# Performance work log

Measured on AMD Instinct MI355X. Metric: run time of the kernel, lower is better.

Reference implementation:

```python
import jax, jax.numpy as jnp
import numpy as np
from functools import partial

# dims matching init_kwargs
H = 512      # hidden_size
F = 2048     # ff_size
NH = 8       # num_heads
NL = 6       # num_layers
V = 1024     # vocab_size
T = 8        # sentence_length
S = 5        # n_sentences_in_paragraph
P = 16       # n_paragraphs_in_article
L = P * S * T          # article_length = 640
N = L + 1              # sequence length used by masks = 641
B = 16                 # batch
HD = H // NH           # head dim
LN_EPS = 1e-5
NEG = -1e9


def _build_mask():
    # pseudo_causal_masks[0] from the torch __init__: causal ~tril plus
    # blocking of within-paragraph sentence-0 key columns.
    a = np.ones((P, S, T, P, S, T), dtype=bool)
    j = np.arange(P)
    a[j, :, :, j, 0, :] = False
    a = a.reshape(L, L)
    causal = ~np.tril(np.ones((N, N), dtype=bool))
    m = causal.copy()
    m[:-1, 1:] = np.logical_and(a, causal[:-1, 1:])
    return m  # True = disallowed


def _build_pe():
    # sinusoidal pe exactly as in __init__ (div_term uses hidden_size in denom)
    pos = np.arange(N, dtype=np.float32)[:, None]
    div = np.exp(np.arange(0, H // 2, dtype=np.float32) * (-np.log(10000.0) / H))
    pe = np.zeros((N, H), dtype=np.float32)
    pe[:, 0::2] = np.sin(pos * div)
    pe[:, 1::2] = np.cos(pos * div)
    return pe


def setup_inputs() -> dict:
    key = jax.random.key(0)
    ks = jax.random.split(key, 12)
    sd = 0.02
    inp = {
        'tokens': jax.random.randint(ks[0], (B, N), 0, V),
        'attn_mask': jnp.asarray(_build_mask()),
        'pe': jnp.asarray(_build_pe()),
        'emb': jax.random.normal(ks[1], (V, H), jnp.float32) * sd,
        'qkv_w': jax.random.normal(ks[2], (NL, 3 * H, H), jnp.float32) * sd,
        'qkv_b': jnp.zeros((NL, 3 * H), jnp.float32),
        'out_w': jax.random.normal(ks[3], (NL, H, H), jnp.float32) * sd,
        'out_b': jnp.zeros((NL, H), jnp.float32),
        'ln1_g': jnp.ones((NL, H), jnp.float32),
        'ln1_b': jnp.zeros((NL, H), jnp.float32),
        'fc1_w': jax.random.normal(ks[4], (NL, F, H), jnp.float32) * sd,
        'fc1_b': jnp.zeros((NL, F), jnp.float32),
        'fc2_w': jax.random.normal(ks[5], (NL, H, F), jnp.float32) * sd,
        'fc2_b': jnp.zeros((NL, H), jnp.float32),
        'ln2_g': jnp.ones((NL, H), jnp.float32),
        'ln2_b': jnp.zeros((NL, H), jnp.float32),
        'lnf_g': jnp.ones((H,), jnp.float32),
        'lnf_b': jnp.zeros((H,), jnp.float32),
        'dep_w': jax.random.normal(ks[6], (V, H), jnp.float32) * sd,
        'dep_b': jnp.zeros((V,), jnp.float32),
    }
    return inp


def _ln(x, g, b):
    m = jnp.mean(x, axis=-1, keepdims=True)
    v = jnp.mean(jnp.square(x - m), axis=-1, keepdims=True)
    return (x - m) * jax.lax.rsqrt(v + LN_EPS) * g + b


def _encoder_layer(x, p, mask):
    qw, qb, ow, ob, g1, b1, w1, bb1, w2, bb2, g2, b2 = p
    Bsz, Nn, _ = x.shape
    qkv = x @ qw.T + qb                                   # [B,N,3H]
    q, k, v = jnp.split(qkv, 3, axis=-1)
    q = q.reshape(Bsz, Nn, NH, HD)
    k = k.reshape(Bsz, Nn, NH, HD)
    v = v.reshape(Bsz, Nn, NH, HD)
    scores = jnp.einsum('bqhd,bkhd->bhqk', q, k) / jnp.sqrt(jnp.asarray(HD, x.dtype))
    scores = jnp.where(mask[None, None], NEG, scores)
    att = jax.nn.softmax(scores, axis=-1)
    o = jnp.einsum('bhqk,bkhd->bqhd', att, v).reshape(Bsz, Nn, H)
    o = o @ ow.T + ob
    x = _ln(x + o, g1, b1)                                # post-LN (torch default)
    f = jax.nn.gelu(x @ w1.T + bb1, approximate=False) @ w2.T + bb2
    return _ln(x + f, g2, b2)


def reference(tokens, attn_mask, pe, emb, qkv_w, qkv_b, out_w, out_b,
              ln1_g, ln1_b, fc1_w, fc1_b, fc2_w, fc2_b, ln2_g, ln2_b,
              lnf_g, lnf_b, dep_w, dep_b):
    x = emb[tokens] + pe[None]                            # [B,N,H]
    layers = (qkv_w, qkv_b, out_w, out_b, ln1_g, ln1_b,
              fc1_w, fc1_b, fc2_w, fc2_b, ln2_g, ln2_b)

    def step(h, p):
        return _encoder_layer(h, p, attn_mask), None

    x, _ = jax.lax.scan(step, x, layers)
    x = _ln(x, lnf_g, lnf_b)
    return x @ dep_w.T + dep_b                            # [B,N,V] logits
```

## Files before the change

### kernel.cpp

```cpp
#include <hip/hip_runtime.h>
#include <stdint.h>

#define NSEQ 641
#define BATCH 16
#define MROWS (BATCH * NSEQ)
#define HID 512
#define FFD 2048
#define NHEAD 8
#define HDIM 64
#define NLAYER 6
#define VOCAB 1024

typedef __bf16 bf16x8 __attribute__((ext_vector_type(8)));
typedef float  f32x4  __attribute__((ext_vector_type(4)));
typedef int    i32x4  __attribute__((ext_vector_type(4)));
typedef short  s16x8  __attribute__((ext_vector_type(8)));
typedef short  s16x4  __attribute__((ext_vector_type(4)));

__device__ __forceinline__ uint32_t swz(uint32_t b) { return b ^ (((b >> 7) & 7u) << 4); }

__device__ __forceinline__ unsigned short f2bf(float f) {
  uint32_t u = __builtin_bit_cast(uint32_t, f);
  u += 0x7FFFu + ((u >> 16) & 1u);
  return (unsigned short)(u >> 16);
}

__device__ __forceinline__ void gload16(const void* g, void* l) {
  __builtin_amdgcn_global_load_lds(
      (const __attribute__((address_space(1))) uint32_t*)g,
      (__attribute__((address_space(3))) uint32_t*)l, 16, 0, 0);
}

__device__ __forceinline__ bf16x8 ld_lds16(const void* p) {
  return __builtin_bit_cast(bf16x8, *(const i32x4*)p);
}

__global__ void cvt_kernel(const float* __restrict__ in,
                           unsigned short* __restrict__ out, int n) {
  int i = (blockIdx.x * 256 + threadIdx.x) * 4;
  if (i >= n) return;
  f32x4 v = *(const f32x4*)(in + i);
  s16x4 o;
  o[0] = (short)f2bf(v[0]); o[1] = (short)f2bf(v[1]);
  o[2] = (short)f2bf(v[2]); o[3] = (short)f2bf(v[3]);
  *(s16x4*)(out + i) = o;
}

__global__ void embed_kernel(const int* __restrict__ tok,
                             const float* __restrict__ emb,
                             const float* __restrict__ pe,
                             float* __restrict__ x,
                             unsigned short* __restrict__ xb) {
  int m = blockIdx.x;
  int n = m % NSEQ;
  int t = tok[m];
  int h = threadIdx.x * 4;
  f32x4 e = *(const f32x4*)(emb + (size_t)t * HID + h);
  f32x4 p = *(const f32x4*)(pe + (size_t)n * HID + h);
  f32x4 v = e + p;
  *(f32x4*)(x + (size_t)m * HID + h) = v;
  s16x4 o;
  o[0] = (short)f2bf(v[0]); o[1] = (short)f2bf(v[1]);
  o[2] = (short)f2bf(v[2]); o[3] = (short)f2bf(v[3]);
  *(s16x4*)(xb + (size_t)m * HID + h) = o;
}

__global__ __launch_bounds__(256) void ln_kernel(
    const float* __restrict__ in, const float* __restrict__ gg,
    const float* __restrict__ bb, float* __restrict__ xo,
    unsigned short* __restrict__ xbo, int rows) {
  int row = blockIdx.x * 4 + (threadIdx.x >> 6);
  if (row >= rows) return;
  int lane = threadIdx.x & 63;
  const float* p = in + (size_t)row * HID + lane * 8;
  f32x4 a0 = *(const f32x4*)p;
  f32x4 a1 = *(const f32x4*)(p + 4);
  float s = a0[0] + a0[1] + a0[2] + a0[3] + a1[0] + a1[1] + a1[2] + a1[3];
#pragma unroll
  for (int o = 32; o; o >>= 1) s += __shfl_xor(s, o);
  float mean = s * (1.0f / HID);
  float vs = 0.f;
#pragma unroll
  for (int j = 0; j < 4; ++j) { float d = a0[j] - mean; vs += d * d; }
#pragma unroll
  for (int j = 0; j < 4; ++j) { float d = a1[j] - mean; vs += d * d; }
#pragma unroll
  for (int o = 32; o; o >>= 1) vs += __shfl_xor(vs, o);
  float rstd = rsqrtf(vs * (1.0f / HID) + 1e-5f);
  f32x4 g0 = *(const f32x4*)(gg + lane * 8);
  f32x4 g1 = *(const f32x4*)(gg + lane * 8 + 4);
  f32x4 b0 = *(const f32x4*)(bb + lane * 8);
  f32x4 b1 = *(const f32x4*)(bb + lane * 8 + 4);
  f32x4 y0, y1;
  s16x8 ob;
#pragma unroll
  for (int j = 0; j < 4; ++j) {
    y0[j] = (a0[j] - mean) * rstd * g0[j] + b0[j];
    y1[j] = (a1[j] - mean) * rstd * g1[j] + b1[j];
    ob[j] = (short)f2bf(y0[j]);
    ob[j + 4] = (short)f2bf(y1[j]);
  }
  float* xp = xo + (size_t)row * HID + lane * 8;
  *(f32x4*)xp = y0;
  *(f32x4*)(xp + 4) = y1;
  *(s16x8*)(xbo + (size_t)row * HID + lane * 8) = ob;
}

enum { EPI_QKV = 0, EPI_GELU = 1, EPI_RESID = 2, EPI_F32OUT = 3 };

template <int EPI>
__global__ __launch_bounds__(256, 2) void gemm_bt(
    const unsigned short* __restrict__ A, const unsigned short* __restrict__ W,
    const float* __restrict__ bias, const float* __restrict__ resid,
    void* __restrict__ out0, void* __restrict__ out1, void* __restrict__ out2,
    int M, int N, int K) {
  __shared__ char sm[32768];
  const int tid = threadIdx.x, lane = tid & 63, wid = tid >> 6;
  const int wr = wid >> 1, wc = wid & 1;
  const int m0 = blockIdx.y * 128, n0 = blockIdx.x * 128;
  f32x4 acc[4][4] = {};
  const uint32_t Pbase = wid * 4096;

  for (int kt = 0; kt < K; kt += 64) {
#pragma unroll
    for (int i = 0; i < 4; ++i) {
      uint32_t P = Pbase + i * 1024 + lane * 16;
      uint32_t L = swz(P);
      int row = (int)(L >> 7);
      uint32_t kb = L & 127u;
      int ma = m0 + row; if (ma >= M) ma = M - 1;
      gload16((const char*)A + ((size_t)ma * K + kt) * 2 + kb, sm + Pbase + i * 1024);
      gload16((const char*)W + ((size_t)(n0 + row) * K + kt) * 2 + kb,
              sm + 16384 + Pbase + i * 1024);
    }
    __syncthreads();
#pragma unroll
    for (int kk = 0; kk < 2; ++kk) {
      bf16x8 af[4], bfr[4];
#pragma unroll
      for (int mi = 0; mi < 4; ++mi) {
        int row = wr * 64 + mi * 16 + (lane & 15);
        af[mi] = ld_lds16(sm + swz((uint32_t)row * 128 + kk * 64 + ((lane >> 4) << 4)));
      }
#pragma unroll
      for (int ni = 0; ni < 4; ++ni) {
        int row = wc * 64 + ni * 16 + (lane & 15);
        bfr[ni] = ld_lds16(sm + 16384 + swz((uint32_t)row * 128 + kk * 64 + ((lane >> 4) << 4)));
      }
#pragma unroll
      for (int mi = 0; mi < 4; ++mi)
#pragma unroll
        for (int ni = 0; ni < 4; ++ni)
          acc[mi][ni] = __builtin_amdgcn_mfma_f32_16x16x32_bf16(af[mi], bfr[ni], acc[mi][ni], 0, 0, 0);
    }
    __syncthreads();
  }

#pragma unroll
  for (int mi = 0; mi < 4; ++mi) {
#pragma unroll
    for (int g = 0; g < 4; ++g) {
      int m = m0 + wr * 64 + mi * 16 + (lane >> 4) * 4 + g;
      if (m >= M) continue;
      int bbq = 0, nn = 0;
      if (EPI == EPI_QKV) { bbq = m / NSEQ; nn = m - bbq * NSEQ; }
#pragma unroll
      for (int ni = 0; ni < 4; ++ni) {
        int c = n0 + wc * 64 + ni * 16 + (lane & 15);
        float v = acc[mi][ni][g] + bias[c];
        if (EPI == EPI_QKV) {
          int which = c >> 9, hh = (c >> 6) & 7, d = c & 63;
          unsigned short* dst = which == 0 ? (unsigned short*)out0
                              : which == 1 ? (unsigned short*)out1
                                           : (unsigned short*)out2;
          dst[(((size_t)bbq * NHEAD + hh) * NSEQ + nn) * HDIM + d] = f2bf(v);
        } else if (EPI == EPI_GELU) {
          v = 0.5f * v * (1.0f + erff(v * 0.70710678118654752f));
          ((unsigned short*)out0)[(size_t)m * N + c] = f2bf(v);
        } else if (EPI == EPI_RESID) {
          float* o = (float*)out0;
          o[(size_t)m * N + c] = v + resid[(size_t)m * N + c];
        } else {
          ((float*)out0)[(size_t)m * N + c] = v;
        }
      }
    }
  }
}

__global__ __launch_bounds__(256) void attn_kernel(
    const unsigned short* __restrict__ Q, const unsigned short* __restrict__ Kb,
    const unsigned short* __restrict__ V, unsigned short* __restrict__ O) {
  const int qt = blockIdx.x, bh = blockIdx.y;
  const int b = bh >> 3, h = bh & 7;
  const int q0 = qt * 64;
  const int tid = threadIdx.x, lane = tid & 63, w = tid >> 6;
  __shared__ char sK[8192];
  __shared__ char sV[8192];
  __shared__ char sP[4][2048];

  const size_t base = (size_t)bh * (NSEQ * HDIM);

  bf16x8 qf[2];
  {
    int qr = q0 + w * 16 + (lane & 15);
    if (qr > NSEQ - 1) qr = NSEQ - 1;
#pragma unroll
    for (int kk = 0; kk < 2; ++kk)
      qf[kk] = __builtin_bit_cast(
          bf16x8, *(const i32x4*)(Q + base + (size_t)qr * HDIM + kk * 32 + ((lane >> 4) << 3)));
  }

  f32x4 acc[4] = {};
  float mrow[4] = {-1e30f, -1e30f, -1e30f, -1e30f};
  float lrow[4] = {0.f, 0.f, 0.f, 0.f};
  const int qrow_base = q0 + w * 16 + ((lane >> 4) << 2);

  int nkt = (q0 + 103) / 64 + 1;
  if (nkt > 11) nkt = 11;

  for (int kt = 0; kt < nkt; ++kt) {
    const int k0 = kt * 64;
#pragma unroll
    for (int i = 0; i < 2; ++i) {
      uint32_t P = w * 2048 + i * 1024 + lane * 16;
      uint32_t L = swz(P);
      int row = (int)(L >> 7);
      uint32_t kbyte = L & 127u;
      int kr = k0 + row; if (kr > NSEQ - 1) kr = NSEQ - 1;
      gload16((const char*)(Kb + base + (size_t)kr * HDIM) + kbyte, sK + w * 2048 + i * 1024);
    }
#pragma unroll
    for (int it = 0; it < 2; ++it) {
      int idx = it * 256 + tid;
      int key = idx >> 3, d0 = (idx & 7) << 3;
      int kr = k0 + key; if (kr > NSEQ - 1) kr = NSEQ - 1;
      s16x8 vv = *(const s16x8*)(V + base + (size_t)kr * HDIM + d0);
#pragma unroll
      for (int j = 0; j < 8; ++j)
        *(short*)(sV + swz((uint32_t)(d0 + j) * 128 + key * 2)) = vv[j];
    }
    __syncthreads();

    f32x4 s[4] = {};
#pragma unroll
    for (int nt = 0; nt < 4; ++nt) {
#pragma unroll
      for (int kk = 0; kk < 2; ++kk) {
        int row = nt * 16 + (lane & 15);
        bf16x8 kf = ld_lds16(sK + swz((uint32_t)row * 128 + kk * 64 + ((lane >> 4) << 4)));
        s[nt] = __builtin_amdgcn_mfma_f32_16x16x32_bf16(qf[kk], kf, s[nt], 0, 0, 0);
      }
    }
    float mx[4];
#pragma unroll
    for (int g = 0; g < 4; ++g) {
      int q = qrow_base + g;
      int p = q / 40;
      int lo = p * 40 + 1, hi = p * 40 + 8;
      float best = -1e30f;
#pragma unroll
      for (int nt = 0; nt < 4; ++nt) {
        int k = k0 + nt * 16 + (lane & 15);
        bool ok = ((k <= q) || (k >= lo && k <= hi)) && (k < NSEQ);
        float v = ok ? s[nt][g] * 0.125f : -1e30f;
        s[nt][g] = v;
        best = fmaxf(best, v);
      }
      mx[g] = best;
    }
#pragma unroll
    for (int o = 1; o < 16; o <<= 1)
#pragma unroll
      for (int g = 0; g < 4; ++g) mx[g] = fmaxf(mx[g], __shfl_xor(mx[g], o));

    float alpha[4], rs[4];
#pragma unroll
    for (int g = 0; g < 4; ++g) {
      float mnew = fmaxf(mrow[g], mx[g]);
      alpha[g] = __expf(mrow[g] - mnew);
      mrow[g] = mnew;
      float sum = 0.f;
#pragma unroll
      for (int nt = 0; nt < 4; ++nt) {
        float pv = __expf(s[nt][g] - mnew);
        s[nt][g] = pv;
        sum += pv;
      }
      rs[g] = sum;
    }
#pragma unroll
    for (int o = 1; o < 16; o <<= 1)
#pragma unroll
      for (int g = 0; g < 4; ++g) rs[g] += __shfl_xor(rs[g], o);
#pragma unroll
    for (int g = 0; g < 4; ++g) {
      lrow[g] = lrow[g] * alpha[g] + rs[g];
#pragma unroll
      for (int nt = 0; nt < 4; ++nt) acc[nt][g] *= alpha[g];
    }

#pragma unroll
    for (int g = 0; g < 4; ++g) {
      int row = ((lane >> 4) << 2) + g;
#pragma unroll
      for (int nt = 0; nt < 4; ++nt) {
        int col = nt * 16 + (lane & 15);
        *(short*)(sP[w] + swz((uint32_t)row * 128 + col * 2)) = (short)f2bf(s[nt][g]);
      }
    }
#pragma unroll
    for (int kk = 0; kk < 2; ++kk) {
      int rowp = lane & 15;
      bf16x8 pa = ld_lds16(sP[w] + swz((uint32_t)rowp * 128 + kk * 64 + ((lane >> 4) << 4)));
#pragma unroll
      for (int nt = 0; nt < 4; ++nt) {
        int rowv = nt * 16 + (lane & 15);
        bf16x8 vf = ld_lds16(sV + swz((uint32_t)rowv * 128 + kk * 64 + ((lane >> 4) << 4)));
        acc[nt] = __builtin_amdgcn_mfma_f32_16x16x32_bf16(pa, vf, acc[nt], 0, 0, 0);
      }
    }
    __syncthreads();
  }

#pragma unroll
  for (int g = 0; g < 4; ++g) {
    int q = qrow_base + g;
    if (q >= NSEQ) continue;
    float inv = 1.0f / lrow[g];
#pragma unroll
    for (int nt = 0; nt < 4; ++nt) {
      int d = nt * 16 + (lane & 15);
      O[((size_t)b * NSEQ + q) * HID + h * HDIM + d] = f2bf(acc[nt][g] * inv);
    }
  }
}

extern "C" void kernel_launch(void* const* d_in, const int* in_sizes, int n_in,
                              void* d_out, int out_size, void* d_ws, size_t ws_size,
                              hipStream_t stream) {
  const int*   tok   = (const int*)d_in[0];
  const float* pe    = (const float*)d_in[2];
  const float* emb   = (const float*)d_in[3];
  const float* qkv_w = (const float*)d_in[4];
  const float* qkv_b = (const float*)d_in[5];
  const float* out_w = (const float*)d_in[6];
  const float* out_b = (const float*)d_in[7];
  const float* ln1_g = (const float*)d_in[8];
  const float* ln1_b = (const float*)d_in[9];
  const float* fc1_w = (const float*)d_in[10];
  const float* fc1_b = (const float*)d_in[11];
  const float* fc2_w = (const float*)d_in[12];
  const float* fc2_b = (const float*)d_in[13];
  const float* ln2_g = (const float*)d_in[14];
  const float* ln2_b = (const float*)d_in[15];
  const float* lnf_g = (const float*)d_in[16];
  const float* lnf_b = (const float*)d_in[17];
  const float* dep_w = (const float*)d_in[18];
  const float* dep_b = (const float*)d_in[19];

  char* w = (char*)d_ws;
  float* x = (float*)w;            w += (size_t)MROWS * HID * 4;
  unsigned short* xb = (unsigned short*)w; w += (size_t)MROWS * HID * 2;
  unsigned short* qb = (unsigned short*)w; w += (size_t)BATCH * NHEAD * NSEQ * HDIM * 2;
  unsigned short* kb = (unsigned short*)w; w += (size_t)BATCH * NHEAD * NSEQ * HDIM * 2;
  unsigned short* vb = (unsigned short*)w; w += (size_t)BATCH * NHEAD * NSEQ * HDIM * 2;
  unsigned short* ao = (unsigned short*)w; w += (size_t)BATCH * NHEAD * NSEQ * HDIM * 2;
  unsigned short* mid = qb;
  unsigned short* wl_qkv = (unsigned short*)w; w += (size_t)1536 * 512 * 2;
  unsigned short* wl_out = (unsigned short*)w; w += (size_t)512 * 512 * 2;
  unsigned short* wl_fc1 = (unsigned short*)w; w += (size_t)2048 * 512 * 2;
  unsigned short* wl_fc2 = (unsigned short*)w; w += (size_t)512 * 2048 * 2;
  unsigned short* wd     = (unsigned short*)w; w += (size_t)VOCAB * 512 * 2;

  cvt_kernel<<<dim3((VOCAB * 512) / 1024), 256, 0, stream>>>(dep_w, wd, VOCAB * 512);
  embed_kernel<<<dim3(MROWS), 128, 0, stream>>>(tok, emb, pe, x, xb);

  const int lnBlocks = (MROWS + 3) / 4;
  for (int l = 0; l < NLAYER; ++l) {
    cvt_kernel<<<dim3((1536 * 512) / 1024), 256, 0, stream>>>(qkv_w + (size_t)l * 1536 * 512, wl_qkv, 1536 * 512);
    cvt_kernel<<<dim3((512 * 512) / 1024), 256, 0, stream>>>(out_w + (size_t)l * 512 * 512, wl_out, 512 * 512);
    cvt_kernel<<<dim3((2048 * 512) / 1024), 256, 0, stream>>>(fc1_w + (size_t)l * 2048 * 512, wl_fc1, 2048 * 512);
    cvt_kernel<<<dim3((512 * 2048) / 1024), 256, 0, stream>>>(fc2_w + (size_t)l * 512 * 2048, wl_fc2, 512 * 2048);

    gemm_bt<EPI_QKV><<<dim3(12, 81), 256, 0, stream>>>(
        xb, wl_qkv, qkv_b + l * 1536, nullptr, qb, kb, vb, MROWS, 1536, 512);
    attn_kernel<<<dim3(11, 128), 256, 0, stream>>>(qb, kb, vb, ao);
    gemm_bt<EPI_RESID><<<dim3(4, 81), 256, 0, stream>>>(
        ao, wl_out, out_b + l * 512, x, x, nullptr, nullptr, MROWS, 512, 512);
    ln_kernel<<<dim3(lnBlocks), 256, 0, stream>>>(x, ln1_g + l * 512, ln1_b + l * 512, x, xb, MROWS);
    gemm_bt<EPI_GELU><<<dim3(16, 81), 256, 0, stream>>>(
        xb, wl_fc1, fc1_b + l * 2048, nullptr, mid, nullptr, nullptr, MROWS, 2048, 512);
    gemm_bt<EPI_RESID><<<dim3(4, 81), 256, 0, stream>>>(
        mid, wl_fc2, fc2_b + l * 512, x, x, nullptr, nullptr, MROWS, 512, 2048);
    ln_kernel<<<dim3(lnBlocks), 256, 0, stream>>>(x, ln2_g + l * 512, ln2_b + l * 512, x, xb, MROWS);
  }

  ln_kernel<<<dim3(lnBlocks), 256, 0, stream>>>(x, lnf_g, lnf_b, x, xb, MROWS);
  gemm_bt<EPI_F32OUT><<<dim3(8, 81), 256, 0, stream>>>(
      xb, wd, dep_b, nullptr, d_out, nullptr, nullptr, MROWS, VOCAB, 512);
}
```

Baseline: 1.598 ms.

## Pre-transpose V into padded layout and batch weight conversions upfront

Adds a vtrans kernel that writes V transposed into a [bh][d][KPAD] buffer, so the attention kernel can load V tiles with async global-to-LDS copies instead of scattered per-element LDS stores. When workspace allows, it also converts all layers' weights to bf16 in a few large launches before the layer loop instead of four small conversions per layer. This adds one extra kernel launch and an extra V read/write pass per layer, and uses more workspace.

New measurement: 1.507 ms. -5.7%, faster.

```diff
diff --git a/kernel.cpp b/kernel.cpp
--- a/kernel.cpp
+++ b/kernel.cpp
@@ -10,6 +10,7 @@
 #define HDIM 64
 #define NLAYER 6
 #define VOCAB 1024
+#define KPAD 704
 
 typedef __bf16 bf16x8 __attribute__((ext_vector_type(8)));
 typedef float  f32x4  __attribute__((ext_vector_type(4)));
@@ -104,6 +105,37 @@
   *(f32x4*)xp = y0;
   *(f32x4*)(xp + 4) = y1;
   *(s16x8*)(xbo + (size_t)row * HID + lane * 8) = ob;
+}
+
+__global__ __launch_bounds__(256) void vtrans_kernel(
+    const unsigned short* __restrict__ V, unsigned short* __restrict__ vT) {
+  const int kt = blockIdx.x;
+  const int bh = blockIdx.y;
+  const int k0 = kt * 64;
+  const int tid = threadIdx.x;
+  __shared__ unsigned short lds[64][68];
+  const size_t src = (size_t)bh * (NSEQ * HDIM);
+#pragma unroll
+  for (int it = 0; it < 2; ++it) {
+    int k = it * 32 + (tid >> 3);
+    int d0 = (tid & 7) * 8;
+    int kr = k0 + k;
+    s16x8 v = {};
+    if (kr < NSEQ) v = *(const s16x8*)(V + src + (size_t)kr * HDIM + d0);
+    *(s16x8*)&lds[k][d0] = v;
+  }
+  __syncthreads();
+  const int d = tid & 63;
+  const int w = tid >> 6;
+  const size_t dst = ((size_t)bh * 64 + d) * KPAD + k0;
+#pragma unroll
+  for (int it = 0; it < 2; ++it) {
+    int kc = w + it * 4;
+    s16x8 o;
+#pragma unroll
+    for (int i = 0; i < 8; ++i) o[i] = lds[kc * 8 + i][d];
+    *(s16x8*)(vT + dst + kc * 8) = o;
+  }
 }
 
 enum { EPI_QKV = 0, EPI_GELU = 1, EPI_RESID = 2, EPI_F32OUT = 3 };
@@ -190,31 +222,33 @@
 
 __global__ __launch_bounds__(256) void attn_kernel(
     const unsigned short* __restrict__ Q, const unsigned short* __restrict__ Kb,
-    const unsigned short* __restrict__ V, unsigned short* __restrict__ O) {
+    const unsigned short* __restrict__ vT, unsigned short* __restrict__ O) {
   const int qt = blockIdx.x, bh = blockIdx.y;
   const int b = bh >> 3, h = bh & 7;
   const int q0 = qt * 64;
   const int tid = threadIdx.x, lane = tid & 63, w = tid >> 6;
+  const int lg = lane >> 4, lc = lane & 15;
   __shared__ char sK[8192];
   __shared__ char sV[8192];
   __shared__ char sP[4][2048];
 
   const size_t base = (size_t)bh * (NSEQ * HDIM);
+  const size_t baseT = (size_t)bh * (HDIM * KPAD);
 
   bf16x8 qf[2];
   {
-    int qr = q0 + w * 16 + (lane & 15);
+    int qr = q0 + w * 16 + lc;
     if (qr > NSEQ - 1) qr = NSEQ - 1;
 #pragma unroll
     for (int kk = 0; kk < 2; ++kk)
       qf[kk] = __builtin_bit_cast(
-          bf16x8, *(const i32x4*)(Q + base + (size_t)qr * HDIM + kk * 32 + ((lane >> 4) << 3)));
+          bf16x8, *(const i32x4*)(Q + base + (size_t)qr * HDIM + kk * 32 + (lg << 3)));
   }
 
   f32x4 acc[4] = {};
   float mrow[4] = {-1e30f, -1e30f, -1e30f, -1e30f};
   float lrow[4] = {0.f, 0.f, 0.f, 0.f};
-  const int qrow_base = q0 + w * 16 + ((lane >> 4) << 2);
+  const int qrow_base = q0 + w * 16 + (lg << 2);
 
   int nkt = (q0 + 103) / 64 + 1;
   if (nkt > 11) nkt = 11;
@@ -231,14 +265,13 @@
       gload16((const char*)(Kb + base + (size_t)kr * HDIM) + kbyte, sK + w * 2048 + i * 1024);
     }
 #pragma unroll
-    for (int it = 0; it < 2; ++it) {
-      int idx = it * 256 + tid;
-      int key = idx >> 3, d0 = (idx & 7) << 3;
-      int kr = k0 + key; if (kr > NSEQ - 1) kr = NSEQ - 1;
-      s16x8 vv = *(const s16x8*)(V + base + (size_t)kr * HDIM + d0);
-#pragma unroll
-      for (int j = 0; j < 8; ++j)
-        *(short*)(sV + swz((uint32_t)(d0 + j) * 128 + key * 2)) = vv[j];
+    for (int i = 0; i < 2; ++i) {
+      uint32_t P = w * 2048 + i * 1024 + lane * 16;
+      uint32_t L = swz(P);
+      int drow = (int)(L >> 7);
+      uint32_t kbyte = L & 127u;
+      gload16((const char*)(vT + baseT + (size_t)drow * KPAD + k0) + kbyte,
+              sV + w * 2048 + i * 1024);
     }
     __syncthreads();
 
@@ -247,8 +280,8 @@
     for (int nt = 0; nt < 4; ++nt) {
 #pragma unroll
       for (int kk = 0; kk < 2; ++kk) {
-        int row = nt * 16 + (lane & 15);
-        bf16x8 kf = ld_lds16(sK + swz((uint32_t)row * 128 + kk * 64 + ((lane >> 4) << 4)));
+        int row = nt * 16 + lc;
+        bf16x8 kf = ld_lds16(sK + swz((uint32_t)row * 128 + kk * 64 + (lg << 4)));
         s[nt] = __builtin_amdgcn_mfma_f32_16x16x32_bf16(qf[kk], kf, s[nt], 0, 0, 0);
       }
     }
@@ -261,7 +294,7 @@
       float best = -1e30f;
 #pragma unroll
       for (int nt = 0; nt < 4; ++nt) {
-        int k = k0 + nt * 16 + (lane & 15);
+        int k = k0 + nt * 16 + lc;
         bool ok = ((k <= q) || (k >= lo && k <= hi)) && (k < NSEQ);
         float v = ok ? s[nt][g] * 0.125f : -1e30f;
         s[nt][g] = v;
@@ -302,21 +335,20 @@
 
 #pragma unroll
     for (int g = 0; g < 4; ++g) {
-      int row = ((lane >> 4) << 2) + g;
+      int row = (lg << 2) + g;
 #pragma unroll
       for (int nt = 0; nt < 4; ++nt) {
-        int col = nt * 16 + (lane & 15);
+        int col = nt * 16 + lc;
         *(short*)(sP[w] + swz((uint32_t)row * 128 + col * 2)) = (short)f2bf(s[nt][g]);
       }
     }
 #pragma unroll
     for (int kk = 0; kk < 2; ++kk) {
-      int rowp = lane & 15;
-      bf16x8 pa = ld_lds16(sP[w] + swz((uint32_t)rowp * 128 + kk * 64 + ((lane >> 4) << 4)));
+      bf16x8 pa = ld_lds16(sP[w] + swz((uint32_t)lc * 128 + kk * 64 + (lg << 4)));
 #pragma unroll
       for (int nt = 0; nt < 4; ++nt) {
-        int rowv = nt * 16 + (lane & 15);
-        bf16x8 vf = ld_lds16(sV + swz((uint32_t)rowv * 128 + kk * 64 + ((lane >> 4) << 4)));
+        int rowv = nt * 16 + lc;
+        bf16x8 vf = ld_lds16(sV + swz((uint32_t)rowv * 128 + kk * 64 + (lg << 4)));
         acc[nt] = __builtin_amdgcn_mfma_f32_16x16x32_bf16(pa, vf, acc[nt], 0, 0, 0);
       }
     }
@@ -330,7 +362,7 @@
     float inv = 1.0f / lrow[g];
 #pragma unroll
     for (int nt = 0; nt < 4; ++nt) {
-      int d = nt * 16 + (lane & 15);
+      int d = nt * 16 + lc;
       O[((size_t)b * NSEQ + q) * HID + h * HDIM + d] = f2bf(acc[nt][g] * inv);
     }
   }
@@ -359,6 +391,12 @@
   const float* dep_w = (const float*)d_in[18];
   const float* dep_b = (const float*)d_in[19];
 
+  const size_t SZ_QKV = (size_t)1536 * 512;
+  const size_t SZ_OUT = (size_t)512 * 512;
+  const size_t SZ_FC1 = (size_t)2048 * 512;
+  const size_t SZ_FC2 = (size_t)512 * 2048;
+  const size_t SZ_DEP = (size_t)VOCAB * 512;
+
   char* w = (char*)d_ws;
   float* x = (float*)w;            w += (size_t)MROWS * HID * 4;
   unsigned short* xb = (unsigned short*)w; w += (size_t)MROWS * HID * 2;
@@ -367,32 +405,60 @@
   unsigned short* vb = (unsigned short*)w; w += (size_t)BATCH * NHEAD * NSEQ * HDIM * 2;
   unsigned short* ao = (unsigned short*)w; w += (size_t)BATCH * NHEAD * NSEQ * HDIM * 2;
   unsigned short* mid = qb;
-  unsigned short* wl_qkv = (unsigned short*)w; w += (size_t)1536 * 512 * 2;
-  unsigned short* wl_out = (unsigned short*)w; w += (size_t)512 * 512 * 2;
-  unsigned short* wl_fc1 = (unsigned short*)w; w += (size_t)2048 * 512 * 2;
-  unsigned short* wl_fc2 = (unsigned short*)w; w += (size_t)512 * 2048 * 2;
-  unsigned short* wd     = (unsigned short*)w; w += (size_t)VOCAB * 512 * 2;
-
-  cvt_kernel<<<dim3((VOCAB * 512) / 1024), 256, 0, stream>>>(dep_w, wd, VOCAB * 512);
+  unsigned short* vT = (unsigned short*)w; w += (size_t)BATCH * NHEAD * HDIM * KPAD * 2;
+
+  size_t used = (size_t)(w - (char*)d_ws);
+  size_t all_w_bytes = (NLAYER * (SZ_QKV + SZ_OUT + SZ_FC1 + SZ_FC2) + SZ_DEP) * 2;
+  bool upfront = ws_size >= used + all_w_bytes;
+
+  unsigned short *wq_all, *wo_all, *w1_all, *w2_all, *wd;
+  if (upfront) {
+    wq_all = (unsigned short*)w; w += NLAYER * SZ_QKV * 2;
+    wo_all = (unsigned short*)w; w += NLAYER * SZ_OUT * 2;
+    w1_all = (unsigned short*)w; w += NLAYER * SZ_FC1 * 2;
+    w2_all = (unsigned short*)w; w += NLAYER * SZ_FC2 * 2;
+    wd     = (unsigned short*)w; w += SZ_DEP * 2;
+    cvt_kernel<<<dim3((NLAYER * SZ_QKV) / 1024), 256, 0, stream>>>(qkv_w, wq_all, NLAYER * SZ_QKV);
+    cvt_kernel<<<dim3((NLAYER * SZ_OUT) / 1024), 256, 0, stream>>>(out_w, wo_all, NLAYER * SZ_OUT);
+    cvt_kernel<<<dim3((NLAYER * SZ_FC1) / 1024), 256, 0, stream>>>(fc1_w, w1_all, NLAYER * SZ_FC1);
+    cvt_kernel<<<dim3((NLAYER * SZ_FC2) / 1024), 256, 0, stream>>>(fc2_w, w2_all, NLAYER * SZ_FC2);
+    cvt_kernel<<<dim3(SZ_DEP / 1024), 256, 0, stream>>>(dep_w, wd, SZ_DEP);
+  } else {
+    wq_all = (unsigned short*)w; w += SZ_QKV * 2;
+    wo_all = (unsigned short*)w; w += SZ_OUT * 2;
+    w1_all = (unsigned short*)w; w += SZ_FC1 * 2;
+    w2_all = (unsigned short*)w; w += SZ_FC2 * 2;
+    wd     = (unsigned short*)w; w += SZ_DEP * 2;
+    cvt_kernel<<<dim3(SZ_DEP / 1024), 256, 0, stream>>>(dep_w, wd, SZ_DEP);
+  }
+
   embed_kernel<<<dim3(MROWS), 128, 0, stream>>>(tok, emb, pe, x, xb);
 
   const int lnBlocks = (MROWS + 3) / 4;
   for (int l = 0; l < NLAYER; ++l) {
-    cvt_kernel<<<dim3((1536 * 512) / 1024), 256, 0, stream>>>(qkv_w + (size_t)l * 1536 * 512, wl_qkv, 1536 * 512);
-    cvt_kernel<<<dim3((512 * 512) / 1024), 256, 0, stream>>>(out_w + (size_t)l * 512 * 512, wl_out, 512 * 512);
-    cvt_kernel<<<dim3((2048 * 512) / 1024), 256, 0, stream>>>(fc1_w + (size_t)l * 2048 * 512, wl_fc1, 2048 * 512);
-    cvt_kernel<<<dim3((512 * 2048) / 1024), 256, 0, stream>>>(fc2_w + (size_t)l * 512 * 2048, wl_fc2, 512 * 2048);
+    unsigned short *wq, *wo, *w1, *w2;
+    if (upfront) {
+      wq = wq_all + l * SZ_QKV; wo = wo_all + l * SZ_OUT;
+      w1 = w1_all + l * SZ_FC1; w2 = w2_all + l * SZ_FC2;
+    } else {
+      wq = wq_all; wo = wo_all; w1 = w1_all; w2 = w2_all;
+      cvt_kernel<<<dim3(SZ_QKV / 1024), 256, 0, stream>>>(qkv_w + l * SZ_QKV, wq, SZ_QKV);
+      cvt_kernel<<<dim3(SZ_OUT / 1024), 256, 0, stream>>>(out_w + l * SZ_OUT, wo, SZ_OUT);
+      cvt_kernel<<<dim3(SZ_FC1 / 1024), 256, 0, stream>>>(fc1_w + l * SZ_FC1, w1, SZ_FC1);
+      cvt_kernel<<<dim3(SZ_FC2 / 1024), 256, 0, stream>>>(fc2_w + l * SZ_FC2, w2, SZ_FC2);
+    }
 
     gemm_bt<EPI_QKV><<<dim3(12, 81), 256, 0, stream>>>(
-        xb, wl_qkv, qkv_b + l * 1536, nullptr, qb, kb, vb, MROWS, 1536, 512);
-    attn_kernel<<<dim3(11, 128), 256, 0, stream>>>(qb, kb, vb, ao);
+        xb, wq, qkv_b + l * 1536, nullptr, qb, kb, vb, MROWS, 1536, 512);
+    vtrans_kernel<<<dim3(11, 128), 256, 0, stream>>>(vb, vT);
+    attn_kernel<<<dim3(11, 128), 256, 0, stream>>>(qb, kb, vT, ao);
     gemm_bt<EPI_RESID><<<dim3(4, 81), 256, 0, stream>>>(
-        ao, wl_out, out_b + l * 512, x, x, nullptr, nullptr, MROWS, 512, 512);
+        ao, wo, out_b + l * 512, x, x, nullptr, nullptr, MROWS, 512, 512);
     ln_kernel<<<dim3(lnBlocks), 256, 0, stream>>>(x, ln1_g + l * 512, ln1_b + l * 512, x, xb, MROWS);
     gemm_bt<EPI_GELU><<<dim3(16, 81), 256, 0, stream>>>(
-        xb, wl_fc1, fc1_b + l * 2048, nullptr, mid, nullptr, nullptr, MROWS, 2048, 512);
+        xb, w1, fc1_b + l * 2048, nullptr, mid, nullptr, nullptr, MROWS, 2048, 512);
     gemm_bt<EPI_RESID><<<dim3(4, 81), 256, 0, stream>>>(
-        mid, wl_fc2, fc2_b + l * 512, x, x, nullptr, nullptr, MROWS, 512, 2048);
+        mid, w2, fc2_b + l * 512, x, x, nullptr, nullptr, MROWS, 512, 2048);
     ln_kernel<<<dim3(lnBlocks), 256, 0, stream>>>(x, ln2_g + l * 512, ln2_b + l * 512, x, xb, MROWS);
   }
 
```
